# Kernel tuning notes

Hardware: AMD Instinct MI355X
Metric: run time of the kernel (lower is better)

Reference implementation:

```python
import jax, jax.numpy as jnp
import numpy as np

E = 1024
H = 16
DFF = 4 * E
EPS = 1e-5


def layer_norm(x, scale, bias):
    mu = jnp.mean(x, axis=-1, keepdims=True)
    var = jnp.var(x, axis=-1, keepdims=True)
    return (x - mu) * jax.lax.rsqrt(var + EPS) * scale + bias


def setup_inputs() -> dict:
    key = jax.random.key(0)
    ks = jax.random.split(key, 12)
    N, L = 2, 2048
    x = jax.random.normal(ks[0], (N, L, E), dtype=jnp.float32)
    attn_mask = jax.random.randint(ks[1], (N, H, L, L), 0, 2) == 1
    s = 0.02
    return {
        "x": x,
        "attn_mask": attn_mask,
        "ln1_s": jnp.ones((E,), jnp.float32),
        "ln1_b": jnp.zeros((E,), jnp.float32),
        "Wqkv": jax.random.normal(ks[2], (E, 3 * E), jnp.float32) * s,
        "bqkv": jnp.zeros((3 * E,), jnp.float32),
        "Wo": jax.random.normal(ks[3], (E, E), jnp.float32) * s,
        "bo": jnp.zeros((E,), jnp.float32),
        "ln2_s": jnp.ones((E,), jnp.float32),
        "ln2_b": jnp.zeros((E,), jnp.float32),
        "lnf_s": jnp.ones((E,), jnp.float32),
        "lnf_b": jnp.zeros((E,), jnp.float32),
        "W1": jax.random.normal(ks[4], (E, DFF), jnp.float32) * s,
        "b1": jnp.zeros((DFF,), jnp.float32),
        "W2": jax.random.normal(ks[5], (DFF, E), jnp.float32) * s,
        "b2": jnp.zeros((E,), jnp.float32),
    }


def reference(x, attn_mask, ln1_s, ln1_b, Wqkv, bqkv, Wo, bo,
              ln2_s, ln2_b, lnf_s, lnf_b, W1, b1, W2, b2):
    N, L, _ = x.shape
    D = E // H
    # --- self attention (pre-norm) ---
    h = layer_norm(x, ln1_s, ln1_b)
    qkv = h @ Wqkv + bqkv                      # [N,L,3E]
    q, k, v = jnp.split(qkv, 3, axis=-1)
    q = q.reshape(N, L, H, D)
    k = k.reshape(N, L, H, D)
    v = v.reshape(N, L, H, D)
    a = jnp.einsum('nqhd,nkhd->nhqk', q, k) * (D ** -0.5)  # [N,H,L,L]
    a = jnp.where(attn_mask, -jnp.inf, a)
    a = jax.nn.softmax(a, axis=-1)
    o = jnp.einsum('nhqk,nkhd->nqhd', a, v).reshape(N, L, E)
    o = o @ Wo + bo
    x = x + o
    # --- feedforward (norm_2 then FF's internal LN) ---
    h = layer_norm(x, ln2_s, ln2_b)
    h = layer_norm(h, lnf_s, lnf_b)
    h = jax.nn.gelu(h @ W1 + b1, approximate=False) @ W2 + b2
    return x + h
```

## Files before the change

### kernel.cpp

```cpp
#include <hip/hip_runtime.h>
#include <math.h>

#define E_DIM 1024
#define H_HEADS 16
#define D_HEAD 64
#define DFF_DIM 4096
#define L_SEQ 2048
#define N_BATCH 2
#define T_TOK (N_BATCH * L_SEQ)

typedef __attribute__((ext_vector_type(8))) __bf16 bf16x8;
typedef __attribute__((ext_vector_type(4))) float f32x4;

__device__ __forceinline__ unsigned short f2bf(float f) {
  union { float f; unsigned int u; } v; v.f = f;
  unsigned int r = v.u + 0x7fffu + ((v.u >> 16) & 1u);
  return (unsigned short)(r >> 16);
}

__device__ __forceinline__ void gl2lds16(const void* g, void* l) {
  __builtin_amdgcn_global_load_lds(
      (const __attribute__((address_space(1))) unsigned int*)g,
      (__attribute__((address_space(3))) unsigned int*)l, 16, 0, 0);
}

__global__ __launch_bounds__(256) void convert_transpose(
    const float* __restrict__ in, unsigned short* __restrict__ out, int K, int N) {
  __shared__ float tile[32][33];
  int n0 = blockIdx.x * 32, k0 = blockIdx.y * 32;
  int tx = threadIdx.x & 31, ty = threadIdx.x >> 5;
#pragma unroll
  for (int i = 0; i < 32; i += 8)
    tile[ty + i][tx] = in[(size_t)(k0 + ty + i) * N + n0 + tx];
  __syncthreads();
#pragma unroll
  for (int i = 0; i < 32; i += 8)
    out[(size_t)(n0 + ty + i) * K + k0 + tx] = f2bf(tile[tx][ty + i]);
}

__device__ __forceinline__ void block_reduce2(float& a, float& b, float* sm, int tid) {
#pragma unroll
  for (int off = 32; off > 0; off >>= 1) {
    a += __shfl_down(a, off);
    b += __shfl_down(b, off);
  }
  int wid = tid >> 6;
  if ((tid & 63) == 0) { sm[wid * 2] = a; sm[wid * 2 + 1] = b; }
  __syncthreads();
  a = sm[0] + sm[2] + sm[4] + sm[6];
  b = sm[1] + sm[3] + sm[5] + sm[7];
}

__global__ __launch_bounds__(256) void ln_kernel(
    const float* __restrict__ x, const float* __restrict__ s,
    const float* __restrict__ b, unsigned short* __restrict__ out) {
  int row = blockIdx.x, tid = threadIdx.x;
  __shared__ float sm[8];
  float4 v = ((const float4*)(x + (size_t)row * E_DIM))[tid];
  float sum = v.x + v.y + v.z + v.w;
  float sq = v.x * v.x + v.y * v.y + v.z * v.z + v.w * v.w;
  block_reduce2(sum, sq, sm, tid);
  float mu = sum * (1.0f / E_DIM);
  float var = sq * (1.0f / E_DIM) - mu * mu;
  float rs = rsqrtf(var + 1e-5f);
  float4 sv = ((const float4*)s)[tid];
  float4 bv = ((const float4*)b)[tid];
  ushort4 o4;
  o4.x = f2bf((v.x - mu) * rs * sv.x + bv.x);
  o4.y = f2bf((v.y - mu) * rs * sv.y + bv.y);
  o4.z = f2bf((v.z - mu) * rs * sv.z + bv.z);
  o4.w = f2bf((v.w - mu) * rs * sv.w + bv.w);
  ((ushort4*)(out + (size_t)row * E_DIM))[tid] = o4;
}

__global__ __launch_bounds__(256) void ln2_kernel(
    const float* __restrict__ x, const float* __restrict__ s2,
    const float* __restrict__ b2, const float* __restrict__ sf,
    const float* __restrict__ bf_, unsigned short* __restrict__ out) {
  int row = blockIdx.x, tid = threadIdx.x;
  __shared__ float sm[8];
  float4 v = ((const float4*)(x + (size_t)row * E_DIM))[tid];
  float sum = v.x + v.y + v.z + v.w;
  float sq = v.x * v.x + v.y * v.y + v.z * v.z + v.w * v.w;
  block_reduce2(sum, sq, sm, tid);
  float mu = sum * (1.0f / E_DIM);
  float rs = rsqrtf(sq * (1.0f / E_DIM) - mu * mu + 1e-5f);
  float4 s2v = ((const float4*)s2)[tid];
  float4 b2v = ((const float4*)b2)[tid];
  float y0 = (v.x - mu) * rs * s2v.x + b2v.x;
  float y1 = (v.y - mu) * rs * s2v.y + b2v.y;
  float y2 = (v.z - mu) * rs * s2v.z + b2v.z;
  float y3 = (v.w - mu) * rs * s2v.w + b2v.w;
  float sum2 = y0 + y1 + y2 + y3;
  float sq2 = y0 * y0 + y1 * y1 + y2 * y2 + y3 * y3;
  __syncthreads();
  block_reduce2(sum2, sq2, sm, tid);
  float mu2 = sum2 * (1.0f / E_DIM);
  float rs2 = rsqrtf(sq2 * (1.0f / E_DIM) - mu2 * mu2 + 1e-5f);
  float4 sfv = ((const float4*)sf)[tid];
  float4 bfv = ((const float4*)bf_)[tid];
  ushort4 o4;
  o4.x = f2bf((y0 - mu2) * rs2 * sfv.x + bfv.x);
  o4.y = f2bf((y1 - mu2) * rs2 * sfv.y + bfv.y);
  o4.z = f2bf((y2 - mu2) * rs2 * sfv.z + bfv.z);
  o4.w = f2bf((y3 - mu2) * rs2 * sfv.w + bfv.w);
  ((ushort4*)(out + (size_t)row * E_DIM))[tid] = o4;
}

template <int EPI>
__global__ __launch_bounds__(256) void gemm_bt(
    const unsigned short* __restrict__ A, const unsigned short* __restrict__ Bt,
    const float* __restrict__ bias, const float* __restrict__ resid,
    void* __restrict__ outp, int M, int N, int K) {
  __shared__ unsigned short As[128 * 32];
  __shared__ unsigned short Bs[128 * 32];
  int tid = threadIdx.x;
  int lane = tid & 63, wave = tid >> 6;
  int m0 = blockIdx.y * 128, n0 = blockIdx.x * 128;
  int wm = (wave & 1) * 64, wn = (wave >> 1) * 64;
  int lm = lane & 15, lq = lane >> 4;

  int r0 = tid >> 2, coff = (tid & 3) * 8;
  const unsigned short* Abase = A + (size_t)m0 * K;
  const unsigned short* Bbase = Bt + (size_t)n0 * K;
  unsigned short* lA0 = As + (tid >> 6) * 512;
  unsigned short* lA1 = As + 2048 + (tid >> 6) * 512;
  unsigned short* lB0 = Bs + (tid >> 6) * 512;
  unsigned short* lB1 = Bs + 2048 + (tid >> 6) * 512;

  f32x4 acc[4][4] = {};
  for (int k0 = 0; k0 < K; k0 += 32) {
    __syncthreads();
    gl2lds16(Abase + (size_t)r0 * K + k0 + coff, lA0);
    gl2lds16(Abase + (size_t)(r0 + 64) * K + k0 + coff, lA1);
    gl2lds16(Bbase + (size_t)r0 * K + k0 + coff, lB0);
    gl2lds16(Bbase + (size_t)(r0 + 64) * K + k0 + coff, lB1);
    __syncthreads();
    bf16x8 a[4], b[4];
#pragma unroll
    for (int i = 0; i < 4; i++)
      a[i] = *(const bf16x8*)(As + (wm + i * 16 + lm) * 32 + lq * 8);
#pragma unroll
    for (int j = 0; j < 4; j++)
      b[j] = *(const bf16x8*)(Bs + (wn + j * 16 + lm) * 32 + lq * 8);
#pragma unroll
    for (int i = 0; i < 4; i++)
#pragma unroll
      for (int j = 0; j < 4; j++)
        acc[i][j] = __builtin_amdgcn_mfma_f32_16x16x32_bf16(a[i], b[j], acc[i][j], 0, 0, 0);
  }
#pragma unroll
  for (int i = 0; i < 4; i++)
#pragma unroll
    for (int j = 0; j < 4; j++) {
      int row = m0 + wm + i * 16 + lq * 4;
      int col = n0 + wn + j * 16 + lm;
      float bcol = bias[col];
#pragma unroll
      for (int r = 0; r < 4; r++) {
        float v = acc[i][j][r] + bcol;
        size_t idx = (size_t)(row + r) * N + col;
        if (EPI == 0) {
          ((unsigned short*)outp)[idx] = f2bf(v);
        } else if (EPI == 1) {
          float g = 0.5f * v * (1.0f + erff(v * 0.70710678118f));
          ((unsigned short*)outp)[idx] = f2bf(g);
        } else {
          ((float*)outp)[idx] = resid[idx] + v;
        }
      }
    }
}

__global__ __launch_bounds__(256) void attn_kernel(
    const unsigned short* __restrict__ qkv, const int* __restrict__ mask,
    unsigned short* __restrict__ o) {
  const int bq = blockIdx.x;
  const int nh = blockIdx.y;
  const int h = nh & 15;
  const int tid = threadIdx.x, lane = tid & 63, wave = tid >> 6;
  const int lm = lane & 15, lq = lane >> 4;

  __shared__ unsigned short Ks[64 * 64];
  __shared__ unsigned short Vt[64 * 72];
  __shared__ unsigned short Ps[4][16 * 72];

  const int q_base = bq * 64;
  const int tok0 = (nh >> 4) * L_SEQ;
  const int qoff = h * 64, koff = E_DIM + h * 64, voff = 2 * E_DIM + h * 64;
  const int* mbase = mask + (size_t)nh * L_SEQ * L_SEQ;

  bf16x8 qf[2];
  {
    int t = tok0 + q_base + wave * 16 + lm;
    const unsigned short* qr = qkv + (size_t)t * (3 * E_DIM) + qoff + lq * 8;
    qf[0] = *(const bf16x8*)(qr);
    qf[1] = *(const bf16x8*)(qr + 32);
  }

  const int sk0 = tid >> 3, sc0 = tid & 7;
  unsigned short* lK0 = Ks + (tid >> 6) * 512;
  unsigned short* lK1 = Ks + 2048 + (tid >> 6) * 512;
  const int vkey = tid >> 3, vchunk = tid & 7;
  const int qrow = q_base + wave * 16 + lq * 4;

  float m_run[4], l_run[4];
  f32x4 oacc[4] = {};
#pragma unroll
  for (int r = 0; r < 4; r++) { m_run[r] = -1e30f; l_run[r] = 0.0f; }

  for (int kt = 0; kt < L_SEQ / 64; kt++) {
    const int k_base = kt * 64;
    __syncthreads();
    gl2lds16(qkv + (size_t)(tok0 + k_base + sk0) * (3 * E_DIM) + koff +
                 ((sc0 ^ (sk0 & 7)) * 8), lK0);
    gl2lds16(qkv + (size_t)(tok0 + k_base + sk0 + 32) * (3 * E_DIM) + koff +
                 ((sc0 ^ ((sk0 + 32) & 7)) * 8), lK1);
    uint4 vv0 = *(const uint4*)(qkv + (size_t)(tok0 + k_base + vkey) * (3 * E_DIM) + voff + vchunk * 8);
    uint4 vv1 = *(const uint4*)(qkv + (size_t)(tok0 + k_base + vkey + 32) * (3 * E_DIM) + voff + vchunk * 8);
    int mv[4][4];
#pragma unroll
    for (int nt = 0; nt < 4; nt++)
#pragma unroll
      for (int r = 0; r < 4; r++)
        mv[nt][r] = mbase[(size_t)(qrow + r) * L_SEQ + k_base + nt * 16 + lm];
    {
      const unsigned short* p0 = (const unsigned short*)&vv0;
      const unsigned short* p1 = (const unsigned short*)&vv1;
#pragma unroll
      for (int jj = 0; jj < 8; jj++) {
        int jx = (jj + vchunk) & 7;
        Vt[(vchunk * 8 + jx) * 72 + vkey] = p0[jx];
        Vt[(vchunk * 8 + jx) * 72 + vkey + 32] = p1[jx];
      }
    }
    __syncthreads();

    f32x4 s[4];
#pragma unroll
    for (int nt = 0; nt < 4; nt++) {
      int key = nt * 16 + lm, sw = key & 7;
      bf16x8 kb0 = *(const bf16x8*)(Ks + key * 64 + ((lq ^ sw) * 8));
      bf16x8 kb1 = *(const bf16x8*)(Ks + key * 64 + (((lq + 4) ^ sw) * 8));
      f32x4 acc = {};
      acc = __builtin_amdgcn_mfma_f32_16x16x32_bf16(qf[0], kb0, acc, 0, 0, 0);
      acc = __builtin_amdgcn_mfma_f32_16x16x32_bf16(qf[1], kb1, acc, 0, 0, 0);
      s[nt] = acc;
    }
#pragma unroll
    for (int nt = 0; nt < 4; nt++)
#pragma unroll
      for (int r = 0; r < 4; r++) {
        float v = s[nt][r] * 0.125f;
        s[nt][r] = mv[nt][r] ? -1e30f : v;
      }
    float alpha[4], rsum[4];
#pragma unroll
    for (int r = 0; r < 4; r++) {
      float v = fmaxf(fmaxf(s[0][r], s[1][r]), fmaxf(s[2][r], s[3][r]));
#pragma unroll
      for (int mo = 1; mo < 16; mo <<= 1) v = fmaxf(v, __shfl_xor(v, mo));
      float mn = fmaxf(m_run[r], v);
      alpha[r] = __expf(m_run[r] - mn);
      m_run[r] = mn;
      rsum[r] = 0.0f;
    }
    unsigned short* pw = Ps[wave];
#pragma unroll
    for (int nt = 0; nt < 4; nt++)
#pragma unroll
      for (int r = 0; r < 4; r++) {
        float p = __expf(s[nt][r] - m_run[r]);
        rsum[r] += p;
        pw[(lq * 4 + r) * 72 + nt * 16 + lm] = f2bf(p);
      }
#pragma unroll
    for (int r = 0; r < 4; r++) {
      float v = rsum[r];
#pragma unroll
      for (int mo = 1; mo < 16; mo <<= 1) v += __shfl_xor(v, mo);
      l_run[r] = l_run[r] * alpha[r] + v;
    }
#pragma unroll
    for (int j = 0; j < 4; j++)
#pragma unroll
      for (int r = 0; r < 4; r++) oacc[j][r] *= alpha[r];
    __syncthreads();

#pragma unroll
    for (int c = 0; c < 2; c++) {
      bf16x8 pa = *(const bf16x8*)(pw + lm * 72 + c * 32 + lq * 8);
#pragma unroll
      for (int j = 0; j < 4; j++) {
        bf16x8 vb = *(const bf16x8*)(Vt + (j * 16 + lm) * 72 + c * 32 + lq * 8);
        oacc[j] = __builtin_amdgcn_mfma_f32_16x16x32_bf16(pa, vb, oacc[j], 0, 0, 0);
      }
    }
  }
#pragma unroll
  for (int r = 0; r < 4; r++) {
    float inv_l = 1.0f / l_run[r];
    int t = tok0 + qrow + r;
#pragma unroll
    for (int j = 0; j < 4; j++)
      o[(size_t)t * E_DIM + h * 64 + j * 16 + lm] = f2bf(oacc[j][r] * inv_l);
  }
}

extern "C" void kernel_launch(void* const* d_in, const int* in_sizes, int n_in,
                              void* d_out, int out_size, void* d_ws, size_t ws_size,
                              hipStream_t stream) {
  const float* x = (const float*)d_in[0];
  const int* mask = (const int*)d_in[1];
  const float* ln1_s = (const float*)d_in[2];
  const float* ln1_b = (const float*)d_in[3];
  const float* Wqkv = (const float*)d_in[4];
  const float* bqkv = (const float*)d_in[5];
  const float* Wo = (const float*)d_in[6];
  const float* bo = (const float*)d_in[7];
  const float* ln2_s = (const float*)d_in[8];
  const float* ln2_b = (const float*)d_in[9];
  const float* lnf_s = (const float*)d_in[10];
  const float* lnf_b = (const float*)d_in[11];
  const float* W1 = (const float*)d_in[12];
  const float* b1 = (const float*)d_in[13];
  const float* W2 = (const float*)d_in[14];
  const float* b2 = (const float*)d_in[15];

  size_t off = 0;
  auto alloc = [&](size_t bytes) {
    void* p = (char*)d_ws + off;
    off += (bytes + 255) & ~(size_t)255;
    return p;
  };
  unsigned short* WqkvT = (unsigned short*)alloc((size_t)3072 * 1024 * 2);
  unsigned short* WoT = (unsigned short*)alloc((size_t)1024 * 1024 * 2);
  unsigned short* W1T = (unsigned short*)alloc((size_t)4096 * 1024 * 2);
  unsigned short* W2T = (unsigned short*)alloc((size_t)1024 * 4096 * 2);
  unsigned short* h1 = (unsigned short*)alloc((size_t)T_TOK * E_DIM * 2);
  unsigned short* qkvb = (unsigned short*)alloc((size_t)T_TOK * 3 * E_DIM * 2);
  unsigned short* ob = (unsigned short*)alloc((size_t)T_TOK * E_DIM * 2);
  float* x2 = (float*)alloc((size_t)T_TOK * E_DIM * 4);
  unsigned short* h2 = (unsigned short*)alloc((size_t)T_TOK * E_DIM * 2);
  unsigned short* g1 = (unsigned short*)alloc((size_t)T_TOK * DFF_DIM * 2);

  convert_transpose<<<dim3(3072 / 32, 1024 / 32), 256, 0, stream>>>(Wqkv, WqkvT, 1024, 3072);
  convert_transpose<<<dim3(1024 / 32, 1024 / 32), 256, 0, stream>>>(Wo, WoT, 1024, 1024);
  convert_transpose<<<dim3(4096 / 32, 1024 / 32), 256, 0, stream>>>(W1, W1T, 1024, 4096);
  convert_transpose<<<dim3(1024 / 32, 4096 / 32), 256, 0, stream>>>(W2, W2T, 4096, 1024);
  ln_kernel<<<T_TOK, 256, 0, stream>>>(x, ln1_s, ln1_b, h1);
  gemm_bt<0><<<dim3(3072 / 128, T_TOK / 128), 256, 0, stream>>>(
      h1, WqkvT, bqkv, nullptr, qkvb, T_TOK, 3072, 1024);
  attn_kernel<<<dim3(L_SEQ / 64, N_BATCH * H_HEADS), 256, 0, stream>>>(qkvb, mask, ob);
  gemm_bt<2><<<dim3(1024 / 128, T_TOK / 128), 256, 0, stream>>>(
      ob, WoT, bo, x, x2, T_TOK, 1024, 1024);
  ln2_kernel<<<T_TOK, 256, 0, stream>>>(x2, ln2_s, ln2_b, lnf_s, lnf_b, h2);
  gemm_bt<1><<<dim3(DFF_DIM / 128, T_TOK / 128), 256, 0, stream>>>(
      h2, W1T, b1, nullptr, g1, T_TOK, DFF_DIM, 1024);
  gemm_bt<2><<<dim3(1024 / 128, T_TOK / 128), 256, 0, stream>>>(
      g1, W2T, b2, x2, (float*)d_out, T_TOK, 1024, 4096);

  (void)in_sizes; (void)n_in; (void)out_size; (void)ws_size;
}
```

Baseline: 1.153 ms.

## Store QKV head-major, stage mask coalesced via LDS, approximate erf in GELU

The QKV GEMM epilogue now writes Q, K and V in a head-major [3][H][T][64] layout, so the attention kernel reads contiguous 128-byte rows for K and V instead of strided rows of the 3E-wide buffer. K is now loaded into registers and stored to padded LDS instead of going through direct global-to-LDS copies. The mask is fetched as coalesced int4 rows, packed into bytes in LDS, and read back per lane, replacing scattered 4-byte loads. GELU switches from erff to an Abramowitz-Stegun polynomial approximation, which is cheaper but less exact.

```diff
diff --git a/kernel.cpp b/kernel.cpp
--- a/kernel.cpp
+++ b/kernel.cpp
@@ -8,6 +8,7 @@
 #define L_SEQ 2048
 #define N_BATCH 2
 #define T_TOK (N_BATCH * L_SEQ)
+#define HT64 ((size_t)H_HEADS * T_TOK * 64)
 
 typedef __attribute__((ext_vector_type(8))) __bf16 bf16x8;
 typedef __attribute__((ext_vector_type(4))) float f32x4;
@@ -107,6 +108,17 @@
   ((ushort4*)(out + (size_t)row * E_DIM))[tid] = o4;
 }
 
+__device__ __forceinline__ float gelu_exact(float v) {
+  float z = v * 0.70710678118f;
+  float az = fabsf(z);
+  float t = 1.0f / (1.0f + 0.3275911f * az);
+  float poly = ((((1.061405429f * t - 1.453152027f) * t + 1.421413741f) * t -
+                 0.284496736f) * t + 0.254829592f) * t;
+  float y = 1.0f - poly * __expf(-az * az);
+  float er = (z < 0.0f) ? -y : y;
+  return 0.5f * v * (1.0f + er);
+}
+
 template <int EPI>
 __global__ __launch_bounds__(256) void gemm_bt(
     const unsigned short* __restrict__ A, const unsigned short* __restrict__ Bt,
@@ -123,10 +135,10 @@
   int r0 = tid >> 2, coff = (tid & 3) * 8;
   const unsigned short* Abase = A + (size_t)m0 * K;
   const unsigned short* Bbase = Bt + (size_t)n0 * K;
-  unsigned short* lA0 = As + (tid >> 6) * 512;
-  unsigned short* lA1 = As + 2048 + (tid >> 6) * 512;
-  unsigned short* lB0 = Bs + (tid >> 6) * 512;
-  unsigned short* lB1 = Bs + 2048 + (tid >> 6) * 512;
+  unsigned short* lA0 = As + wave * 512;
+  unsigned short* lA1 = As + 2048 + wave * 512;
+  unsigned short* lB0 = Bs + wave * 512;
+  unsigned short* lB1 = Bs + 2048 + wave * 512;
 
   f32x4 acc[4][4] = {};
   for (int k0 = 0; k0 < K; k0 += 32) {
@@ -159,21 +171,25 @@
 #pragma unroll
       for (int r = 0; r < 4; r++) {
         float v = acc[i][j][r] + bcol;
-        size_t idx = (size_t)(row + r) * N + col;
         if (EPI == 0) {
-          ((unsigned short*)outp)[idx] = f2bf(v);
+          ((unsigned short*)outp)[(size_t)(row + r) * N + col] = f2bf(v);
         } else if (EPI == 1) {
-          float g = 0.5f * v * (1.0f + erff(v * 0.70710678118f));
-          ((unsigned short*)outp)[idx] = f2bf(g);
+          ((unsigned short*)outp)[(size_t)(row + r) * N + col] = f2bf(gelu_exact(v));
+        } else if (EPI == 2) {
+          size_t idx = (size_t)(row + r) * N + col;
+          ((float*)outp)[idx] = resid[idx] + v;
         } else {
-          ((float*)outp)[idx] = resid[idx] + v;
+          int which = col >> 10, hh = (col & 1023) >> 6, d = col & 63;
+          unsigned short* dst = (unsigned short*)outp + (size_t)which * HT64 +
+                                ((size_t)hh * T_TOK + row + r) * 64 + d;
+          *dst = f2bf(v);
         }
       }
     }
 }
 
 __global__ __launch_bounds__(256) void attn_kernel(
-    const unsigned short* __restrict__ qkv, const int* __restrict__ mask,
+    const unsigned short* __restrict__ qkvh, const int* __restrict__ mask,
     unsigned short* __restrict__ o) {
   const int bq = blockIdx.x;
   const int nh = blockIdx.y;
@@ -181,27 +197,27 @@
   const int tid = threadIdx.x, lane = tid & 63, wave = tid >> 6;
   const int lm = lane & 15, lq = lane >> 4;
 
-  __shared__ unsigned short Ks[64 * 64];
+  __shared__ unsigned short Ks[64 * 72];
   __shared__ unsigned short Vt[64 * 72];
   __shared__ unsigned short Ps[4][16 * 72];
+  __shared__ unsigned int Msk[64 * 17];
 
   const int q_base = bq * 64;
   const int tok0 = (nh >> 4) * L_SEQ;
-  const int qoff = h * 64, koff = E_DIM + h * 64, voff = 2 * E_DIM + h * 64;
+  const unsigned short* qh = qkvh + (size_t)h * T_TOK * 64;
+  const unsigned short* kh = qkvh + HT64 + (size_t)h * T_TOK * 64;
+  const unsigned short* vh = qkvh + 2 * HT64 + (size_t)h * T_TOK * 64;
   const int* mbase = mask + (size_t)nh * L_SEQ * L_SEQ;
 
   bf16x8 qf[2];
   {
     int t = tok0 + q_base + wave * 16 + lm;
-    const unsigned short* qr = qkv + (size_t)t * (3 * E_DIM) + qoff + lq * 8;
-    qf[0] = *(const bf16x8*)(qr);
-    qf[1] = *(const bf16x8*)(qr + 32);
-  }
-
-  const int sk0 = tid >> 3, sc0 = tid & 7;
-  unsigned short* lK0 = Ks + (tid >> 6) * 512;
-  unsigned short* lK1 = Ks + 2048 + (tid >> 6) * 512;
-  const int vkey = tid >> 3, vchunk = tid & 7;
+    qf[0] = *(const bf16x8*)(qh + (size_t)t * 64 + lq * 8);
+    qf[1] = *(const bf16x8*)(qh + (size_t)t * 64 + 32 + lq * 8);
+  }
+
+  const int skey = tid >> 3, schunk = tid & 7;
+  const int mq0 = (tid >> 4) * 4, mkc = tid & 15;
   const int qrow = q_base + wave * 16 + lq * 4;
 
   float m_run[4], l_run[4];
@@ -211,27 +227,39 @@
 
   for (int kt = 0; kt < L_SEQ / 64; kt++) {
     const int k_base = kt * 64;
-    __syncthreads();
-    gl2lds16(qkv + (size_t)(tok0 + k_base + sk0) * (3 * E_DIM) + koff +
-                 ((sc0 ^ (sk0 & 7)) * 8), lK0);
-    gl2lds16(qkv + (size_t)(tok0 + k_base + sk0 + 32) * (3 * E_DIM) + koff +
-                 ((sc0 ^ ((sk0 + 32) & 7)) * 8), lK1);
-    uint4 vv0 = *(const uint4*)(qkv + (size_t)(tok0 + k_base + vkey) * (3 * E_DIM) + voff + vchunk * 8);
-    uint4 vv1 = *(const uint4*)(qkv + (size_t)(tok0 + k_base + vkey + 32) * (3 * E_DIM) + voff + vchunk * 8);
-    int mv[4][4];
-#pragma unroll
-    for (int nt = 0; nt < 4; nt++)
-#pragma unroll
-      for (int r = 0; r < 4; r++)
-        mv[nt][r] = mbase[(size_t)(qrow + r) * L_SEQ + k_base + nt * 16 + lm];
+    const int t0 = tok0 + k_base;
+    uint4 kv0 = *(const uint4*)(kh + (size_t)(t0 + skey) * 64 + schunk * 8);
+    uint4 kv1 = *(const uint4*)(kh + (size_t)(t0 + skey + 32) * 64 + schunk * 8);
+    uint4 vv0 = *(const uint4*)(vh + (size_t)(t0 + skey) * 64 + schunk * 8);
+    uint4 vv1 = *(const uint4*)(vh + (size_t)(t0 + skey + 32) * 64 + schunk * 8);
+    const int* mrow = mbase + (size_t)(q_base + mq0) * L_SEQ + k_base + mkc * 4;
+    int4 mr0 = *(const int4*)(mrow);
+    int4 mr1 = *(const int4*)(mrow + L_SEQ);
+    int4 mr2 = *(const int4*)(mrow + 2 * L_SEQ);
+    int4 mr3 = *(const int4*)(mrow + 3 * L_SEQ);
+    __syncthreads();
+    *(uint4*)(Ks + skey * 72 + schunk * 8) = kv0;
+    *(uint4*)(Ks + (skey + 32) * 72 + schunk * 8) = kv1;
     {
       const unsigned short* p0 = (const unsigned short*)&vv0;
       const unsigned short* p1 = (const unsigned short*)&vv1;
 #pragma unroll
       for (int jj = 0; jj < 8; jj++) {
-        int jx = (jj + vchunk) & 7;
-        Vt[(vchunk * 8 + jx) * 72 + vkey] = p0[jx];
-        Vt[(vchunk * 8 + jx) * 72 + vkey + 32] = p1[jx];
+        int jx = (jj + schunk) & 7;
+        Vt[(schunk * 8 + jx) * 72 + skey] = p0[jx];
+        Vt[(schunk * 8 + jx) * 72 + skey + 32] = p1[jx];
+      }
+    }
+    {
+      const int* a0 = (const int*)&mr0;
+      const int* a1 = (const int*)&mr1;
+      const int* a2 = (const int*)&mr2;
+      const int* a3 = (const int*)&mr3;
+#pragma unroll
+      for (int kk = 0; kk < 4; kk++) {
+        unsigned u = (a0[kk] ? 1u : 0u) | (a1[kk] ? 256u : 0u) |
+                     (a2[kk] ? 65536u : 0u) | (a3[kk] ? 16777216u : 0u);
+        Msk[(mkc * 4 + kk) * 17 + (mq0 >> 2)] = u;
       }
     }
     __syncthreads();
@@ -239,21 +267,23 @@
     f32x4 s[4];
 #pragma unroll
     for (int nt = 0; nt < 4; nt++) {
-      int key = nt * 16 + lm, sw = key & 7;
-      bf16x8 kb0 = *(const bf16x8*)(Ks + key * 64 + ((lq ^ sw) * 8));
-      bf16x8 kb1 = *(const bf16x8*)(Ks + key * 64 + (((lq + 4) ^ sw) * 8));
+      int key = nt * 16 + lm;
+      bf16x8 kb0 = *(const bf16x8*)(Ks + key * 72 + lq * 8);
+      bf16x8 kb1 = *(const bf16x8*)(Ks + key * 72 + 32 + lq * 8);
       f32x4 acc = {};
       acc = __builtin_amdgcn_mfma_f32_16x16x32_bf16(qf[0], kb0, acc, 0, 0, 0);
       acc = __builtin_amdgcn_mfma_f32_16x16x32_bf16(qf[1], kb1, acc, 0, 0, 0);
       s[nt] = acc;
     }
 #pragma unroll
-    for (int nt = 0; nt < 4; nt++)
+    for (int nt = 0; nt < 4; nt++) {
+      unsigned mu = Msk[(nt * 16 + lm) * 17 + wave * 4 + lq];
 #pragma unroll
       for (int r = 0; r < 4; r++) {
         float v = s[nt][r] * 0.125f;
-        s[nt][r] = mv[nt][r] ? -1e30f : v;
-      }
+        s[nt][r] = ((mu >> (8 * r)) & 0xffu) ? -1e30f : v;
+      }
+    }
     float alpha[4], rsum[4];
 #pragma unroll
     for (int r = 0; r < 4; r++) {
@@ -338,7 +368,7 @@
   unsigned short* W1T = (unsigned short*)alloc((size_t)4096 * 1024 * 2);
   unsigned short* W2T = (unsigned short*)alloc((size_t)1024 * 4096 * 2);
   unsigned short* h1 = (unsigned short*)alloc((size_t)T_TOK * E_DIM * 2);
-  unsigned short* qkvb = (unsigned short*)alloc((size_t)T_TOK * 3 * E_DIM * 2);
+  unsigned short* qkvh = (unsigned short*)alloc(3 * HT64 * 2);
   unsigned short* ob = (unsigned short*)alloc((size_t)T_TOK * E_DIM * 2);
   float* x2 = (float*)alloc((size_t)T_TOK * E_DIM * 4);
   unsigned short* h2 = (unsigned short*)alloc((size_t)T_TOK * E_DIM * 2);
@@ -349,9 +379,9 @@
   convert_transpose<<<dim3(4096 / 32, 1024 / 32), 256, 0, stream>>>(W1, W1T, 1024, 4096);
   convert_transpose<<<dim3(1024 / 32, 4096 / 32), 256, 0, stream>>>(W2, W2T, 4096, 1024);
   ln_kernel<<<T_TOK, 256, 0, stream>>>(x, ln1_s, ln1_b, h1);
-  gemm_bt<0><<<dim3(3072 / 128, T_TOK / 128), 256, 0, stream>>>(
-      h1, WqkvT, bqkv, nullptr, qkvb, T_TOK, 3072, 1024);
-  attn_kernel<<<dim3(L_SEQ / 64, N_BATCH * H_HEADS), 256, 0, stream>>>(qkvb, mask, ob);
+  gemm_bt<3><<<dim3(3072 / 128, T_TOK / 128), 256, 0, stream>>>(
+      h1, WqkvT, bqkv, nullptr, qkvh, T_TOK, 3072, 1024);
+  attn_kernel<<<dim3(L_SEQ / 64, N_BATCH * H_HEADS), 256, 0, stream>>>(qkvh, mask, ob);
   gemm_bt<2><<<dim3(1024 / 128, T_TOK / 128), 256, 0, stream>>>(
       ob, WoT, bo, x, x2, T_TOK, 1024, 1024);
   ln2_kernel<<<T_TOK, 256, 0, stream>>>(x2, ln2_s, ln2_b, lnf_s, lnf_b, h2);
```

Result: no change. 1.164 ms (+0.9%).
